# Performance work log

Measured on AMD Instinct MI355X. Metric: run time of the kernel, lower is better.

## Reference

```python
import jax, jax.numpy as jnp
import numpy as np

N, D, NUM_CLASSES = 8192, 512, 100

def _col_normalize(z):
    # torch.std default is unbiased (ddof=1)
    mean = z.mean(axis=0)
    std = z.std(axis=0, ddof=1)
    return (z - mean) / std

def setup_inputs() -> dict:
    key = jax.random.key(0)
    k1, k2, k3 = jax.random.split(key, 3)
    z_a = jax.random.normal(k1, (N, D), dtype=jnp.float32)
    z_b = jax.random.normal(k2, (N, D), dtype=jnp.float32)
    labels = jax.random.randint(k3, (N,), 0, NUM_CLASSES, dtype=jnp.int64)
    return {"z_a": z_a, "z_b": z_b, "labels": labels}

def reference(z_a, z_b, labels):
    d = z_a.shape[1]
    z_a_norm = _col_normalize(z_a)
    z_b_norm = _col_normalize(z_b)
    # c: [N, N] cross-correlation between samples
    c = jnp.matmul(z_a_norm, z_b_norm.T) / d
    # m[i, j] = 1 if labels[i] == labels[j] else 0 (replaces per-row loop)
    m = (labels[:, None] == labels[None, :]).astype(c.dtype)
    loss = jnp.sum((c - m) ** 2)
    return loss
```

## Files before the change

### kernel.cpp

```cpp
#include <hip/hip_runtime.h>
#include <math.h>


#define NN 8192
#define DD 512
#define NC 100
#define SPLITK 16
#define NXT 10
#define NTILE 14

#define GA_B    0u
#define GB_B    1048576u
#define RTA_B   2097152u
#define RTB_B   2359296u
#define MUA_B   2621440u
#define MUB_B   2623488u
#define RSA_B   2625536u
#define RSB_B   2627584u
#define CNT_B   2629632u
#define XTA_B   4194304u
#define XTB_B   12582912u
#define MT_B    20971520u
#define PART_B  23068672u

typedef __attribute__((ext_vector_type(8))) short short8;
typedef __attribute__((ext_vector_type(4))) float f32x4;

__constant__ int c_ti[NTILE] = {0,0,0,0,1,1,1,2,2,3, 0,1,2,3};
__constant__ int c_tj[NTILE] = {0,1,2,3,1,2,3,2,3,3, 4,4,4,4};
__constant__ float c_w[NXT]  = {1.f,2.f,2.f,2.f,1.f,2.f,2.f,1.f,2.f,1.f};

#if defined(__has_builtin)
#if __has_builtin(__builtin_amdgcn_global_load_lds)
#define HAVE_GLL 1
#endif
#endif

#ifdef HAVE_GLL
__device__ __forceinline__ void async16(const void* g, void* l) {
    __builtin_amdgcn_global_load_lds(
        (const __attribute__((address_space(1))) void*)g,
        (__attribute__((address_space(3))) void*)l, 16, 0, 0);
}
#endif

__device__ __forceinline__ short f2bf_rne(float f) {
    unsigned int u = __builtin_bit_cast(unsigned int, f);
    u += 0x7fffu + ((u >> 16) & 1u);
    return (short)(u >> 16);
}

__device__ __forceinline__ float block_reduce_sum(float v) {
    __shared__ float red[8];
    int lane = threadIdx.x & 63;
    int wave = threadIdx.x >> 6;
    #pragma unroll
    for (int off = 32; off > 0; off >>= 1) v += __shfl_down(v, off, 64);
    if (lane == 0) red[wave] = v;
    __syncthreads();
    float s = 0.f;
    if (threadIdx.x == 0) {
        int nw = (blockDim.x + 63) >> 6;
        for (int w = 0; w < nw; w++) s += red[w];
    }
    return s;
}

__global__ void k_init(const int* __restrict__ labels, short* __restrict__ MT,
                       float* __restrict__ out) {
    int c = blockIdx.x;
    if (c == 128) { if (threadIdx.x == 0) out[0] = 0.f; return; }
    int t = threadIdx.x;
    unsigned short one = 0x3F80;
    ushort4* dst = (ushort4*)(MT + (size_t)c * NN);
    const int4* lb4 = (const int4*)labels;
    #pragma unroll
    for (int j = 0; j < 8; j++) {
        int i4 = j * 256 + t;
        int4 lb = lb4[i4];
        ushort4 v;
        v.x = (lb.x == c) ? one : (unsigned short)0;
        v.y = (lb.y == c) ? one : (unsigned short)0;
        v.z = (lb.z == c) ? one : (unsigned short)0;
        v.w = (lb.w == c) ? one : (unsigned short)0;
        dst[i4] = v;
    }
}

__global__ __launch_bounds__(256) void k_convT(const float* __restrict__ A,
                                               const float* __restrict__ B,
                                               short* __restrict__ XTa,
                                               short* __restrict__ XTb) {
    __shared__ short LT[64][72];
    int bid = blockIdx.x;
    const float* X = (bid >> 10) ? B : A;
    short* XT = (bid >> 10) ? XTb : XTa;
    int rem = bid & 1023;
    int c0 = (rem >> 7) << 6;
    int k0 = (rem & 127) << 6;
    int t = threadIdx.x;

    int cc = t & 15;
    int kb = t >> 4;
    #pragma unroll
    for (int s = 0; s < 4; s++) {
        int kr = kb + s * 16;
        float4 v = *(const float4*)&X[(size_t)(k0 + kr) * DD + c0 + cc * 4];
        LT[cc * 4 + 0][kr] = f2bf_rne(v.x);
        LT[cc * 4 + 1][kr] = f2bf_rne(v.y);
        LT[cc * 4 + 2][kr] = f2bf_rne(v.z);
        LT[cc * 4 + 3][kr] = f2bf_rne(v.w);
    }
    __syncthreads();
    #pragma unroll
    for (int s = 0; s < 2; s++) {
        int idx = s * 256 + t;
        int orow = idx >> 3;
        int och = idx & 7;
        *(uint4*)&XT[(size_t)(c0 + orow) * NN + k0 + och * 8] =
            *(const uint4*)&LT[orow][och * 8];
    }
}

__global__ __launch_bounds__(256, 2) void k_gram(const short* __restrict__ XTa,
                                                 const short* __restrict__ XTb,
                                                 const short* __restrict__ MT,
                                                 float* __restrict__ part) {
    __shared__ short LA[128 * 64];
    __shared__ short LB[128 * 64];

    int bid = blockIdx.x;
    int mat = bid / (NTILE * SPLITK);
    int r = bid % (NTILE * SPLITK);
    int chunk = r / NTILE;
    int tile = r % NTILE;
    const short* XT = mat ? XTb : XTa;
    int ti = c_ti[tile], tj = c_tj[tile];
    const short* PA = XT + (size_t)ti * 128 * NN;
    const short* PB = (tj < 4) ? (XT + (size_t)tj * 128 * NN) : MT;
    int k0 = chunk * (NN / SPLITK);

    int t = threadIdx.x;
    int wave = t >> 6, lane = t & 63;
    int quad = lane >> 4, l16 = lane & 15;
    int x7 = l16 & 7;
    int wrow = (wave >> 1) * 64, wcol = (wave & 1) * 64;

    int srow = lane >> 3;
    int sc = (lane & 7) ^ srow;

    f32x4 acc[4][4];
    #pragma unroll
    for (int i = 0; i < 4; i++)
        #pragma unroll
        for (int j = 0; j < 4; j++) acc[i][j] = (f32x4)0.f;

    for (int kk = 0; kk < NN / SPLITK; kk += 64) {
        __syncthreads();
        #pragma unroll
        for (int rr = 0; rr < 4; rr++) {
            int seg = wave * 4 + rr;
            int row = seg * 8 + srow;
            const short* ga = PA + (size_t)row * NN + k0 + kk + sc * 8;
            const short* gb = PB + (size_t)row * NN + k0 + kk + sc * 8;
#ifdef HAVE_GLL
            async16(ga, &LA[seg * 512]);
            async16(gb, &LB[seg * 512]);
#else
            uint4 va = *(const uint4*)ga;
            uint4 vb = *(const uint4*)gb;
            *(uint4*)&LA[seg * 512 + lane * 8] = va;
            *(uint4*)&LB[seg * 512 + lane * 8] = vb;
#endif
        }
        __syncthreads();
        #pragma unroll
        for (int ks = 0; ks < 2; ks++) {
            short8 a[4], b[4];
            #pragma unroll
            for (int mt = 0; mt < 4; mt++)
                a[mt] = *(const short8*)&LA[(wrow + mt * 16 + l16) * 64 +
                                            (((ks * 4 + quad) ^ x7) << 3)];
            #pragma unroll
            for (int nt = 0; nt < 4; nt++)
                b[nt] = *(const short8*)&LB[(wcol + nt * 16 + l16) * 64 +
                                            (((ks * 4 + quad) ^ x7) << 3)];
            #pragma unroll
            for (int mt = 0; mt < 4; mt++)
                #pragma unroll
                for (int nt = 0; nt < 4; nt++)
                    acc[mt][nt] = __builtin_amdgcn_mfma_f32_16x16x32_bf16(
                        a[mt], b[nt], acc[mt][nt], 0, 0, 0);
        }
    }

    float* pbase = part + ((size_t)(mat * NTILE + tile) * SPLITK + chunk) * 16384;
    #pragma unroll
    for (int mt = 0; mt < 4; mt++)
        #pragma unroll
        for (int nt = 0; nt < 4; nt++)
            #pragma unroll
            for (int rj = 0; rj < 4; rj++) {
                int rr2 = wrow + mt * 16 + quad * 4 + rj;
                int cc2 = wcol + nt * 16 + l16;
                pbase[rr2 * 128 + cc2] = acc[mt][nt][rj];
            }
}

__global__ void k_gsum(const float* __restrict__ part,
                       float* __restrict__ Ga, float* __restrict__ Gb,
                       float* __restrict__ RTa, float* __restrict__ RTb) {
    int bid = blockIdx.x;
    int mat = bid / (NTILE * 64);
    int rr = bid % (NTILE * 64);
    int tile = rr / 64;
    int e = (rr % 64) * 256 + threadIdx.x;
    const float* p = part + (size_t)(mat * NTILE + tile) * SPLITK * 16384 + e;
    float s = 0.f;
    #pragma unroll
    for (int c = 0; c < SPLITK; c++) s += p[(size_t)c * 16384];
    int rw = e >> 7, cl = e & 127;
    if (tile < NXT) {
        float* G = mat ? Gb : Ga;
        G[(c_ti[tile] * 128 + rw) * DD + c_tj[tile] * 128 + cl] = s;
    } else {
        float* RT = mat ? RTb : RTa;
        RT[cl * DD + (tile - NXT) * 128 + rw] = s;
    }
}

__global__ void k_stats(const float* __restrict__ Ga, const float* __restrict__ Gb,
                        const float* __restrict__ RTa, const float* __restrict__ RTb,
                        const int* __restrict__ labels,
                        float* mu_a, float* mu_b, float* rs_a, float* rs_b,
                        int* counts) {
    if (blockIdx.x == 2) {
        __shared__ int h[NC];
        int t = threadIdx.x;
        if (t < NC) h[t] = 0;
        __syncthreads();
        for (int i = t; i < NN; i += blockDim.x) atomicAdd(&h[labels[i]], 1);
        __syncthreads();
        if (t < NC) counts[t] = h[t];
        return;
    }
    int mat = blockIdx.x;
    int k = threadIdx.x;
    const float* RT = mat ? RTb : RTa;
    const float* G = mat ? Gb : Ga;
    float s = 0.f;
    for (int c = 0; c < 128; c++) s += RT[c * DD + k];
    float mu = s / (float)NN;
    float sumsq = G[k * DD + k];
    float var = (sumsq - (float)NN * mu * mu) / (float)(NN - 1);
    (mat ? mu_b : mu_a)[k] = mu;
    (mat ? rs_b : rs_a)[k] = rsqrtf(var);
}

__global__ void k_term(const float* __restrict__ Ga, const float* __restrict__ Gb,
                       const float* __restrict__ RTa, const float* __restrict__ RTb,
                       const float* __restrict__ mu_a, const float* __restrict__ mu_b,
                       const float* __restrict__ rs_a, const float* __restrict__ rs_b,
                       const int* __restrict__ counts, float* out) {
    int bid = blockIdx.x;
    if (bid < 256) {
        float local = 0.f;
        for (int x = bid * 256 + threadIdx.x; x < NXT * 16384; x += 256 * 256) {
            int tile = x >> 14, e = x & 16383;
            int gi = c_ti[tile] * 128 + (e >> 7);
            int gj = c_tj[tile] * 128 + (e & 127);
            float ga = rs_a[gi] * rs_a[gj] * (Ga[gi * DD + gj] - (float)NN * mu_a[gi] * mu_a[gj]);
            float gb = rs_b[gi] * rs_b[gj] * (Gb[gi * DD + gj] - (float)NN * mu_b[gi] * mu_b[gj]);
            local += c_w[tile] * ga * gb;
        }
        float s = block_reduce_sum(local);
        if (threadIdx.x == 0) atomicAdd(out, s * (1.0f / ((float)DD * (float)DD)));
    } else {
        int c = bid - 256;
        float n = (float)counts[c];
        float local = 0.f;
        for (int k = threadIdx.x; k < DD; k += 256) {
            float ta = rs_a[k] * (RTa[c * DD + k] - n * mu_a[k]);
            float tb = rs_b[k] * (RTb[c * DD + k] - n * mu_b[k]);
            local += ta * tb;
        }
        float s = block_reduce_sum(local);
        if (threadIdx.x == 0) {
            float add = s * (-2.0f / (float)DD);
            if (c == 0) {
                float t3 = 0.f;
                for (int cc = 0; cc < NC; cc++) {
                    float nc = (float)counts[cc];
                    t3 += nc * nc;
                }
                add += t3;
            }
            atomicAdd(out, add);
        }
    }
}

extern "C" void kernel_launch(void* const* d_in, const int* in_sizes, int n_in,
                              void* d_out, int out_size, void* d_ws, size_t ws_size,
                              hipStream_t stream) {
    const float* z_a = (const float*)d_in[0];
    const float* z_b = (const float*)d_in[1];
    const int* labels = (const int*)d_in[2];
    float* out = (float*)d_out;
    char* wsb = (char*)d_ws;

    float* Ga = (float*)(wsb + GA_B);
    float* Gb = (float*)(wsb + GB_B);
    float* RTa = (float*)(wsb + RTA_B);
    float* RTb = (float*)(wsb + RTB_B);
    float* mu_a = (float*)(wsb + MUA_B);
    float* mu_b = (float*)(wsb + MUB_B);
    float* rs_a = (float*)(wsb + RSA_B);
    float* rs_b = (float*)(wsb + RSB_B);
    int* counts = (int*)(wsb + CNT_B);
    short* XTa = (short*)(wsb + XTA_B);
    short* XTb = (short*)(wsb + XTB_B);
    short* MT = (short*)(wsb + MT_B);
    float* part = (float*)(wsb + PART_B);

    hipLaunchKernelGGL(k_init, dim3(129), dim3(256), 0, stream, labels, MT, out);
    hipLaunchKernelGGL(k_convT, dim3(2048), dim3(256), 0, stream, z_a, z_b, XTa, XTb);
    hipLaunchKernelGGL(k_gram, dim3(2 * NTILE * SPLITK), dim3(256), 0, stream,
                       XTa, XTb, MT, part);
    hipLaunchKernelGGL(k_gsum, dim3(2 * NTILE * 64), dim3(256), 0, stream,
                       part, Ga, Gb, RTa, RTb);
    hipLaunchKernelGGL(k_stats, dim3(3), dim3(512), 0, stream,
                       Ga, Gb, RTa, RTb, labels, mu_a, mu_b, rs_a, rs_b, counts);
    hipLaunchKernelGGL(k_term, dim3(356), dim3(256), 0, stream,
                       Ga, Gb, RTa, RTb, mu_a, mu_b, rs_a, rs_b, counts, out);
}
```

Measured before the change: 118.3 us.

## Fold split-K reduction into consumers and compute column sums during transpose

Removes the k_gsum pass: k_stats reads the diagonal partials straight from the split-K buffer, and k_term sums the SPLITK partials inline, with the Gram work spread over more blocks. Column sums for the means are now gathered in k_convT with shared and global atomics, and the label histogram moves into k_init. This drops one launch and the write and re-read of the G and RT matrices. In exchange k_convT uses strided scalar loads with no LDS transpose, and the float atomics make the column sums order-dependent.

```diff
diff --git a/kernel.cpp b/kernel.cpp
--- a/kernel.cpp
+++ b/kernel.cpp
@@ -9,15 +9,12 @@
 #define NXT 10
 #define NTILE 14
 
-#define GA_B    0u
-#define GB_B    1048576u
-#define RTA_B   2097152u
-#define RTB_B   2359296u
-#define MUA_B   2621440u
-#define MUB_B   2623488u
-#define RSA_B   2625536u
-#define RSB_B   2627584u
-#define CNT_B   2629632u
+#define MUA_B   0u
+#define MUB_B   2048u
+#define RSA_B   4096u
+#define RSB_B   6144u
+#define CNT_B   8192u
+#define CS_B    12288u
 #define XTA_B   4194304u
 #define XTB_B   12582912u
 #define MT_B    20971520u
@@ -44,10 +41,10 @@
 }
 #endif
 
-__device__ __forceinline__ short f2bf_rne(float f) {
+__device__ __forceinline__ unsigned short f2bf_rne(float f) {
     unsigned int u = __builtin_bit_cast(unsigned int, f);
     u += 0x7fffu + ((u >> 16) & 1u);
-    return (short)(u >> 16);
+    return (unsigned short)(u >> 16);
 }
 
 __device__ __forceinline__ float block_reduce_sum(float v) {
@@ -67,10 +64,24 @@
 }
 
 __global__ void k_init(const int* __restrict__ labels, short* __restrict__ MT,
+                       float* __restrict__ colsum, int* __restrict__ counts,
                        float* __restrict__ out) {
     int c = blockIdx.x;
-    if (c == 128) { if (threadIdx.x == 0) out[0] = 0.f; return; }
     int t = threadIdx.x;
+    if (c == 128) {
+        __shared__ int h[NC];
+        if (t < NC) h[t] = 0;
+        __syncthreads();
+        for (int i = t; i < NN; i += blockDim.x) atomicAdd(&h[labels[i]], 1);
+        __syncthreads();
+        if (t < NC) counts[t] = h[t];
+        return;
+    }
+    if (c == 129) {
+        for (int i = t; i < 2 * DD; i += blockDim.x) colsum[i] = 0.f;
+        if (t == 0) out[0] = 0.f;
+        return;
+    }
     unsigned short one = 0x3F80;
     ushort4* dst = (ushort4*)(MT + (size_t)c * NN);
     const int4* lb4 = (const int4*)labels;
@@ -90,36 +101,42 @@
 __global__ __launch_bounds__(256) void k_convT(const float* __restrict__ A,
                                                const float* __restrict__ B,
                                                short* __restrict__ XTa,
-                                               short* __restrict__ XTb) {
-    __shared__ short LT[64][72];
-    int bid = blockIdx.x;
-    const float* X = (bid >> 10) ? B : A;
-    short* XT = (bid >> 10) ? XTb : XTa;
-    int rem = bid & 1023;
-    int c0 = (rem >> 7) << 6;
-    int k0 = (rem & 127) << 6;
+                                               short* __restrict__ XTb,
+                                               float* __restrict__ colsum) {
+    int b = blockIdx.x;
+    int mat = b >> 9;
+    int cg = (b >> 6) & 7;
+    int kg = b & 63;
+    const float* X = mat ? B : A;
+    short* XT = mat ? XTb : XTa;
     int t = threadIdx.x;
-
-    int cc = t & 15;
-    int kb = t >> 4;
-    #pragma unroll
-    for (int s = 0; s < 4; s++) {
-        int kr = kb + s * 16;
-        float4 v = *(const float4*)&X[(size_t)(k0 + kr) * DD + c0 + cc * 4];
-        LT[cc * 4 + 0][kr] = f2bf_rne(v.x);
-        LT[cc * 4 + 1][kr] = f2bf_rne(v.y);
-        LT[cc * 4 + 2][kr] = f2bf_rne(v.z);
-        LT[cc * 4 + 3][kr] = f2bf_rne(v.w);
-    }
+    int cl = t & 63;
+    int c = cg * 64 + cl;
+    int k0 = kg * 128 + (t >> 6) * 32;
+
+    const float* src = X + (size_t)k0 * DD + c;
+    short* dst = XT + (size_t)c * NN + k0;
+    float s = 0.f;
+    #pragma unroll
+    for (int j = 0; j < 4; j++) {
+        unsigned int w[4];
+        #pragma unroll
+        for (int q = 0; q < 4; q++) {
+            float v0 = src[(size_t)(j * 8 + q * 2) * DD];
+            float v1 = src[(size_t)(j * 8 + q * 2 + 1) * DD];
+            s += v0 + v1;
+            w[q] = ((unsigned int)f2bf_rne(v1) << 16) | (unsigned int)f2bf_rne(v0);
+        }
+        uint4 vv; vv.x = w[0]; vv.y = w[1]; vv.z = w[2]; vv.w = w[3];
+        *(uint4*)(dst + j * 8) = vv;
+    }
+
+    __shared__ float cs[64];
+    if (t < 64) cs[t] = 0.f;
     __syncthreads();
-    #pragma unroll
-    for (int s = 0; s < 2; s++) {
-        int idx = s * 256 + t;
-        int orow = idx >> 3;
-        int och = idx & 7;
-        *(uint4*)&XT[(size_t)(c0 + orow) * NN + k0 + och * 8] =
-            *(const uint4*)&LT[orow][och * 8];
-    }
+    atomicAdd(&cs[cl], s);
+    __syncthreads();
+    if (t < 64) atomicAdd(&colsum[mat * DD + cg * 64 + t], cs[t]);
 }
 
 __global__ __launch_bounds__(256, 2) void k_gram(const short* __restrict__ XTa,
@@ -207,85 +224,73 @@
             }
 }
 
-__global__ void k_gsum(const float* __restrict__ part,
-                       float* __restrict__ Ga, float* __restrict__ Gb,
-                       float* __restrict__ RTa, float* __restrict__ RTb) {
-    int bid = blockIdx.x;
-    int mat = bid / (NTILE * 64);
-    int rr = bid % (NTILE * 64);
-    int tile = rr / 64;
-    int e = (rr % 64) * 256 + threadIdx.x;
-    const float* p = part + (size_t)(mat * NTILE + tile) * SPLITK * 16384 + e;
-    float s = 0.f;
-    #pragma unroll
-    for (int c = 0; c < SPLITK; c++) s += p[(size_t)c * 16384];
-    int rw = e >> 7, cl = e & 127;
-    if (tile < NXT) {
-        float* G = mat ? Gb : Ga;
-        G[(c_ti[tile] * 128 + rw) * DD + c_tj[tile] * 128 + cl] = s;
-    } else {
-        float* RT = mat ? RTb : RTa;
-        RT[cl * DD + (tile - NXT) * 128 + rw] = s;
-    }
-}
-
-__global__ void k_stats(const float* __restrict__ Ga, const float* __restrict__ Gb,
-                        const float* __restrict__ RTa, const float* __restrict__ RTb,
-                        const int* __restrict__ labels,
-                        float* mu_a, float* mu_b, float* rs_a, float* rs_b,
-                        int* counts) {
-    if (blockIdx.x == 2) {
-        __shared__ int h[NC];
-        int t = threadIdx.x;
-        if (t < NC) h[t] = 0;
-        __syncthreads();
-        for (int i = t; i < NN; i += blockDim.x) atomicAdd(&h[labels[i]], 1);
-        __syncthreads();
-        if (t < NC) counts[t] = h[t];
-        return;
-    }
+__global__ void k_stats(const float* __restrict__ part, const float* __restrict__ colsum,
+                        float* mu_a, float* mu_b, float* rs_a, float* rs_b) {
     int mat = blockIdx.x;
     int k = threadIdx.x;
-    const float* RT = mat ? RTb : RTa;
-    const float* G = mat ? Gb : Ga;
-    float s = 0.f;
-    for (int c = 0; c < 128; c++) s += RT[c * DD + k];
-    float mu = s / (float)NN;
-    float sumsq = G[k * DD + k];
+    const int dmap[4] = {0, 4, 7, 9};
+    int tile = dmap[k >> 7];
+    size_t base = ((size_t)(mat * NTILE + tile) * SPLITK) * 16384 + (size_t)(k & 127) * 129;
+    float sumsq = 0.f;
+    #pragma unroll
+    for (int c = 0; c < SPLITK; c++) sumsq += part[base + (size_t)c * 16384];
+    float mu = colsum[mat * DD + k] / (float)NN;
     float var = (sumsq - (float)NN * mu * mu) / (float)(NN - 1);
     (mat ? mu_b : mu_a)[k] = mu;
     (mat ? rs_b : rs_a)[k] = rsqrtf(var);
 }
 
-__global__ void k_term(const float* __restrict__ Ga, const float* __restrict__ Gb,
-                       const float* __restrict__ RTa, const float* __restrict__ RTb,
+__global__ void k_term(const float* __restrict__ part,
                        const float* __restrict__ mu_a, const float* __restrict__ mu_b,
                        const float* __restrict__ rs_a, const float* __restrict__ rs_b,
                        const int* __restrict__ counts, float* out) {
     int bid = blockIdx.x;
-    if (bid < 256) {
+    int t = threadIdx.x;
+    if (bid < 320) {
+        int tile = bid >> 5;
+        int seg = bid & 31;
+        size_t baseA = ((size_t)(0 * NTILE + tile) * SPLITK) * 16384;
+        size_t baseB = ((size_t)(1 * NTILE + tile) * SPLITK) * 16384;
+        float w = c_w[tile];
         float local = 0.f;
-        for (int x = bid * 256 + threadIdx.x; x < NXT * 16384; x += 256 * 256) {
-            int tile = x >> 14, e = x & 16383;
+        #pragma unroll
+        for (int half = 0; half < 2; half++) {
+            int e = seg * 512 + half * 256 + t;
+            float sA = 0.f, sB = 0.f;
+            #pragma unroll
+            for (int c = 0; c < SPLITK; c++) {
+                sA += part[baseA + (size_t)c * 16384 + e];
+                sB += part[baseB + (size_t)c * 16384 + e];
+            }
             int gi = c_ti[tile] * 128 + (e >> 7);
             int gj = c_tj[tile] * 128 + (e & 127);
-            float ga = rs_a[gi] * rs_a[gj] * (Ga[gi * DD + gj] - (float)NN * mu_a[gi] * mu_a[gj]);
-            float gb = rs_b[gi] * rs_b[gj] * (Gb[gi * DD + gj] - (float)NN * mu_b[gi] * mu_b[gj]);
-            local += c_w[tile] * ga * gb;
+            float ga = rs_a[gi] * rs_a[gj] * (sA - (float)NN * mu_a[gi] * mu_a[gj]);
+            float gb = rs_b[gi] * rs_b[gj] * (sB - (float)NN * mu_b[gi] * mu_b[gj]);
+            local += w * ga * gb;
         }
         float s = block_reduce_sum(local);
-        if (threadIdx.x == 0) atomicAdd(out, s * (1.0f / ((float)DD * (float)DD)));
+        if (t == 0) atomicAdd(out, s * (1.0f / ((float)DD * (float)DD)));
     } else {
-        int c = bid - 256;
+        int c = bid - 320;
         float n = (float)counts[c];
         float local = 0.f;
-        for (int k = threadIdx.x; k < DD; k += 256) {
-            float ta = rs_a[k] * (RTa[c * DD + k] - n * mu_a[k]);
-            float tb = rs_b[k] * (RTb[c * DD + k] - n * mu_b[k]);
+        for (int k = t; k < DD; k += 256) {
+            int tile = NXT + (k >> 7);
+            size_t e = (size_t)(k & 127) * 128 + c;
+            size_t baseA = ((size_t)(0 * NTILE + tile) * SPLITK) * 16384 + e;
+            size_t baseB = ((size_t)(1 * NTILE + tile) * SPLITK) * 16384 + e;
+            float sA = 0.f, sB = 0.f;
+            #pragma unroll
+            for (int ch = 0; ch < SPLITK; ch++) {
+                sA += part[baseA + (size_t)ch * 16384];
+                sB += part[baseB + (size_t)ch * 16384];
+            }
+            float ta = rs_a[k] * (sA - n * mu_a[k]);
+            float tb = rs_b[k] * (sB - n * mu_b[k]);
             local += ta * tb;
         }
         float s = block_reduce_sum(local);
-        if (threadIdx.x == 0) {
+        if (t == 0) {
             float add = s * (-2.0f / (float)DD);
             if (c == 0) {
                 float t3 = 0.f;
@@ -309,28 +314,25 @@
     float* out = (float*)d_out;
     char* wsb = (char*)d_ws;
 
-    float* Ga = (float*)(wsb + GA_B);
-    float* Gb = (float*)(wsb + GB_B);
-    float* RTa = (float*)(wsb + RTA_B);
-    float* RTb = (float*)(wsb + RTB_B);
     float* mu_a = (float*)(wsb + MUA_B);
     float* mu_b = (float*)(wsb + MUB_B);
     float* rs_a = (float*)(wsb + RSA_B);
     float* rs_b = (float*)(wsb + RSB_B);
     int* counts = (int*)(wsb + CNT_B);
+    float* colsum = (float*)(wsb + CS_B);
     short* XTa = (short*)(wsb + XTA_B);
     short* XTb = (short*)(wsb + XTB_B);
     short* MT = (short*)(wsb + MT_B);
     float* part = (float*)(wsb + PART_B);
 
-    hipLaunchKernelGGL(k_init, dim3(129), dim3(256), 0, stream, labels, MT, out);
-    hipLaunchKernelGGL(k_convT, dim3(2048), dim3(256), 0, stream, z_a, z_b, XTa, XTb);
+    hipLaunchKernelGGL(k_init, dim3(130), dim3(256), 0, stream,
+                       labels, MT, colsum, counts, out);
+    hipLaunchKernelGGL(k_convT, dim3(1024), dim3(256), 0, stream,
+                       z_a, z_b, XTa, XTb, colsum);
     hipLaunchKernelGGL(k_gram, dim3(2 * NTILE * SPLITK), dim3(256), 0, stream,
                        XTa, XTb, MT, part);
-    hipLaunchKernelGGL(k_gsum, dim3(2 * NTILE * 64), dim3(256), 0, stream,
-                       part, Ga, Gb, RTa, RTb);
-    hipLaunchKernelGGL(k_stats, dim3(3), dim3(512), 0, stream,
-                       Ga, Gb, RTa, RTb, labels, mu_a, mu_b, rs_a, rs_b, counts);
-    hipLaunchKernelGGL(k_term, dim3(356), dim3(256), 0, stream,
-                       Ga, Gb, RTa, RTb, mu_a, mu_b, rs_a, rs_b, counts, out);
-}
+    hipLaunchKernelGGL(k_stats, dim3(2), dim3(512), 0, stream,
+                       part, colsum, mu_a, mu_b, rs_a, rs_b);
+    hipLaunchKernelGGL(k_term, dim3(420), dim3(256), 0, stream,
+                       part, mu_a, mu_b, rs_a, rs_b, counts, out);
+}
```

Measured after the change: 145.0 us. 22.6% more time.

## Fuse all stages into one cooperative persistent kernel with grid syncs

Applied to the files above, without the earlier changes.

Replaces the six separate launches (init, transpose-convert, gram, split-K reduce, stats, loss terms) with one cooperative kernel of 448 blocks. Stages are separated by grid.sync(), and the earlier stages use grid-stride job loops. The aim is to remove per-launch gaps and tail idle time between the small stages. The trade-offs are the cost of several grid-wide barriers and a larger LDS footprint per block from combining all stages. The Gram term loop now walks the full 512x512 matrix and skips the lower triangle, instead of using the tile table.

```diff
diff --git a/kernel.cpp b/kernel.cpp
--- a/kernel.cpp
+++ b/kernel.cpp
@@ -1,5 +1,8 @@
 #include <hip/hip_runtime.h>
+#include <hip/hip_cooperative_groups.h>
 #include <math.h>
+
+namespace cg = cooperative_groups;
 
 
 #define NN 8192
@@ -8,6 +11,7 @@
 #define SPLITK 16
 #define NXT 10
 #define NTILE 14
+#define GRID 448
 
 #define GA_B    0u
 #define GB_B    1048576u
@@ -44,10 +48,10 @@
 }
 #endif
 
-__device__ __forceinline__ short f2bf_rne(float f) {
+__device__ __forceinline__ unsigned short f2bf_rne(float f) {
     unsigned int u = __builtin_bit_cast(unsigned int, f);
     u += 0x7fffu + ((u >> 16) & 1u);
-    return (short)(u >> 16);
+    return (unsigned short)(u >> 16);
 }
 
 __device__ __forceinline__ float block_reduce_sum(float v) {
@@ -66,226 +70,221 @@
     return s;
 }
 
-__global__ void k_init(const int* __restrict__ labels, short* __restrict__ MT,
-                       float* __restrict__ out) {
-    int c = blockIdx.x;
-    if (c == 128) { if (threadIdx.x == 0) out[0] = 0.f; return; }
-    int t = threadIdx.x;
-    unsigned short one = 0x3F80;
-    ushort4* dst = (ushort4*)(MT + (size_t)c * NN);
-    const int4* lb4 = (const int4*)labels;
-    #pragma unroll
-    for (int j = 0; j < 8; j++) {
-        int i4 = j * 256 + t;
-        int4 lb = lb4[i4];
-        ushort4 v;
-        v.x = (lb.x == c) ? one : (unsigned short)0;
-        v.y = (lb.y == c) ? one : (unsigned short)0;
-        v.z = (lb.z == c) ? one : (unsigned short)0;
-        v.w = (lb.w == c) ? one : (unsigned short)0;
-        dst[i4] = v;
-    }
-}
-
-__global__ __launch_bounds__(256) void k_convT(const float* __restrict__ A,
-                                               const float* __restrict__ B,
-                                               short* __restrict__ XTa,
-                                               short* __restrict__ XTb) {
+__global__ __launch_bounds__(256, 2) void k_fused(
+        const float* __restrict__ A, const float* __restrict__ B,
+        const int* __restrict__ labels,
+        short* __restrict__ XTa, short* __restrict__ XTb, short* __restrict__ MT,
+        float* __restrict__ part,
+        float* __restrict__ Ga, float* __restrict__ Gb,
+        float* __restrict__ RTa, float* __restrict__ RTb,
+        float* __restrict__ mu_a, float* __restrict__ mu_b,
+        float* __restrict__ rs_a, float* __restrict__ rs_b,
+        int* __restrict__ counts, float* __restrict__ out) {
+    cg::grid_group grid = cg::this_grid();
     __shared__ short LT[64][72];
-    int bid = blockIdx.x;
-    const float* X = (bid >> 10) ? B : A;
-    short* XT = (bid >> 10) ? XTb : XTa;
-    int rem = bid & 1023;
-    int c0 = (rem >> 7) << 6;
-    int k0 = (rem & 127) << 6;
-    int t = threadIdx.x;
-
-    int cc = t & 15;
-    int kb = t >> 4;
-    #pragma unroll
-    for (int s = 0; s < 4; s++) {
-        int kr = kb + s * 16;
-        float4 v = *(const float4*)&X[(size_t)(k0 + kr) * DD + c0 + cc * 4];
-        LT[cc * 4 + 0][kr] = f2bf_rne(v.x);
-        LT[cc * 4 + 1][kr] = f2bf_rne(v.y);
-        LT[cc * 4 + 2][kr] = f2bf_rne(v.z);
-        LT[cc * 4 + 3][kr] = f2bf_rne(v.w);
-    }
-    __syncthreads();
-    #pragma unroll
-    for (int s = 0; s < 2; s++) {
-        int idx = s * 256 + t;
-        int orow = idx >> 3;
-        int och = idx & 7;
-        *(uint4*)&XT[(size_t)(c0 + orow) * NN + k0 + och * 8] =
-            *(const uint4*)&LT[orow][och * 8];
-    }
-}
-
-__global__ __launch_bounds__(256, 2) void k_gram(const short* __restrict__ XTa,
-                                                 const short* __restrict__ XTb,
-                                                 const short* __restrict__ MT,
-                                                 float* __restrict__ part) {
     __shared__ short LA[128 * 64];
     __shared__ short LB[128 * 64];
 
-    int bid = blockIdx.x;
-    int mat = bid / (NTILE * SPLITK);
-    int r = bid % (NTILE * SPLITK);
-    int chunk = r / NTILE;
-    int tile = r % NTILE;
-    const short* XT = mat ? XTb : XTa;
-    int ti = c_ti[tile], tj = c_tj[tile];
-    const short* PA = XT + (size_t)ti * 128 * NN;
-    const short* PB = (tj < 4) ? (XT + (size_t)tj * 128 * NN) : MT;
-    int k0 = chunk * (NN / SPLITK);
-
-    int t = threadIdx.x;
-    int wave = t >> 6, lane = t & 63;
-    int quad = lane >> 4, l16 = lane & 15;
-    int x7 = l16 & 7;
-    int wrow = (wave >> 1) * 64, wcol = (wave & 1) * 64;
-
-    int srow = lane >> 3;
-    int sc = (lane & 7) ^ srow;
-
-    f32x4 acc[4][4];
-    #pragma unroll
-    for (int i = 0; i < 4; i++)
+    const int bid = blockIdx.x;
+    const int t = threadIdx.x;
+
+    for (int job = bid; job < 2177; job += GRID) {
+        if (job < 2048) {
+            int mat = job >> 10;
+            const float* X = mat ? B : A;
+            short* XT = mat ? XTb : XTa;
+            int rem = job & 1023;
+            int c0 = (rem >> 7) << 6;
+            int k0 = (rem & 127) << 6;
+            int cc = t & 15;
+            int kb = t >> 4;
+            #pragma unroll
+            for (int s = 0; s < 4; s++) {
+                int kr = kb + s * 16;
+                float4 v = *(const float4*)&X[(size_t)(k0 + kr) * DD + c0 + cc * 4];
+                LT[cc * 4 + 0][kr] = (short)f2bf_rne(v.x);
+                LT[cc * 4 + 1][kr] = (short)f2bf_rne(v.y);
+                LT[cc * 4 + 2][kr] = (short)f2bf_rne(v.z);
+                LT[cc * 4 + 3][kr] = (short)f2bf_rne(v.w);
+            }
+            __syncthreads();
+            #pragma unroll
+            for (int s = 0; s < 2; s++) {
+                int idx = s * 256 + t;
+                int orow = idx >> 3;
+                int och = idx & 7;
+                *(uint4*)&XT[(size_t)(c0 + orow) * NN + k0 + och * 8] =
+                    *(const uint4*)&LT[orow][och * 8];
+            }
+            __syncthreads();
+        } else if (job < 2176) {
+            int c = job - 2048;
+            unsigned short one = 0x3F80;
+            ushort4* dst = (ushort4*)(MT + (size_t)c * NN);
+            const int4* lb4 = (const int4*)labels;
+            #pragma unroll
+            for (int j = 0; j < 8; j++) {
+                int i4 = j * 256 + t;
+                int4 lb = lb4[i4];
+                ushort4 v;
+                v.x = (lb.x == c) ? one : (unsigned short)0;
+                v.y = (lb.y == c) ? one : (unsigned short)0;
+                v.z = (lb.z == c) ? one : (unsigned short)0;
+                v.w = (lb.w == c) ? one : (unsigned short)0;
+                dst[i4] = v;
+            }
+        } else {
+            if (t == 0) out[0] = 0.f;
+        }
+    }
+    grid.sync();
+
+    {
+        int mat = bid / (NTILE * SPLITK);
+        int r = bid % (NTILE * SPLITK);
+        int chunk = r / NTILE;
+        int tile = r % NTILE;
+        const short* XT = mat ? XTb : XTa;
+        int ti = c_ti[tile], tj = c_tj[tile];
+        const short* PA = XT + (size_t)ti * 128 * NN;
+        const short* PB = (tj < 4) ? (XT + (size_t)tj * 128 * NN) : MT;
+        int k0 = chunk * (NN / SPLITK);
+
+        int wave = t >> 6, lane = t & 63;
+        int quad = lane >> 4, l16 = lane & 15;
+        int x7 = l16 & 7;
+        int wrow = (wave >> 1) * 64, wcol = (wave & 1) * 64;
+
+        int srow = lane >> 3;
+        int sc = (lane & 7) ^ srow;
+
+        f32x4 acc[4][4];
         #pragma unroll
-        for (int j = 0; j < 4; j++) acc[i][j] = (f32x4)0.f;
-
-    for (int kk = 0; kk < NN / SPLITK; kk += 64) {
-        __syncthreads();
-        #pragma unroll
-        for (int rr = 0; rr < 4; rr++) {
-            int seg = wave * 4 + rr;
-            int row = seg * 8 + srow;
-            const short* ga = PA + (size_t)row * NN + k0 + kk + sc * 8;
-            const short* gb = PB + (size_t)row * NN + k0 + kk + sc * 8;
+        for (int i = 0; i < 4; i++)
+            #pragma unroll
+            for (int j = 0; j < 4; j++) acc[i][j] = (f32x4)0.f;
+
+        for (int kk = 0; kk < NN / SPLITK; kk += 64) {
+            __syncthreads();
+            #pragma unroll
+            for (int rr = 0; rr < 4; rr++) {
+                int seg = wave * 4 + rr;
+                int row = seg * 8 + srow;
+                const short* ga = PA + (size_t)row * NN + k0 + kk + sc * 8;
+                const short* gb = PB + (size_t)row * NN + k0 + kk + sc * 8;
 #ifdef HAVE_GLL
-            async16(ga, &LA[seg * 512]);
-            async16(gb, &LB[seg * 512]);
+                async16(ga, &LA[seg * 512]);
+                async16(gb, &LB[seg * 512]);
 #else
-            uint4 va = *(const uint4*)ga;
-            uint4 vb = *(const uint4*)gb;
-            *(uint4*)&LA[seg * 512 + lane * 8] = va;
-            *(uint4*)&LB[seg * 512 + lane * 8] = vb;
+                uint4 va = *(const uint4*)ga;
+                uint4 vb = *(const uint4*)gb;
+                *(uint4*)&LA[seg * 512 + lane * 8] = va;
+                *(uint4*)&LB[seg * 512 + lane * 8] = vb;
 #endif
-        }
-        __syncthreads();
-        #pragma unroll
-        for (int ks = 0; ks < 2; ks++) {
-            short8 a[4], b[4];
-            #pragma unroll
-            for (int mt = 0; mt < 4; mt++)
-                a[mt] = *(const short8*)&LA[(wrow + mt * 16 + l16) * 64 +
-                                            (((ks * 4 + quad) ^ x7) << 3)];
-            #pragma unroll
-            for (int nt = 0; nt < 4; nt++)
-                b[nt] = *(const short8*)&LB[(wcol + nt * 16 + l16) * 64 +
-                                            (((ks * 4 + quad) ^ x7) << 3)];
-            #pragma unroll
-            for (int mt = 0; mt < 4; mt++)
+            }
+            __syncthreads();
+            #pragma unroll
+            for (int ks = 0; ks < 2; ks++) {
+                short8 a[4], b[4];
+                #pragma unroll
+                for (int mt = 0; mt < 4; mt++)
+                    a[mt] = *(const short8*)&LA[(wrow + mt * 16 + l16) * 64 +
+                                                (((ks * 4 + quad) ^ x7) << 3)];
                 #pragma unroll
                 for (int nt = 0; nt < 4; nt++)
-                    acc[mt][nt] = __builtin_amdgcn_mfma_f32_16x16x32_bf16(
-                        a[mt], b[nt], acc[mt][nt], 0, 0, 0);
-        }
-    }
-
-    float* pbase = part + ((size_t)(mat * NTILE + tile) * SPLITK + chunk) * 16384;
-    #pragma unroll
-    for (int mt = 0; mt < 4; mt++)
+                    b[nt] = *(const short8*)&LB[(wcol + nt * 16 + l16) * 64 +
+                                                (((ks * 4 + quad) ^ x7) << 3)];
+                #pragma unroll
+                for (int mt = 0; mt < 4; mt++)
+                    #pragma unroll
+                    for (int nt = 0; nt < 4; nt++)
+                        acc[mt][nt] = __builtin_amdgcn_mfma_f32_16x16x32_bf16(
+                            a[mt], b[nt], acc[mt][nt], 0, 0, 0);
+            }
+        }
+
+        float* pbase = part + ((size_t)(mat * NTILE + tile) * SPLITK + chunk) * 16384;
         #pragma unroll
-        for (int nt = 0; nt < 4; nt++)
-            #pragma unroll
-            for (int rj = 0; rj < 4; rj++) {
-                int rr2 = wrow + mt * 16 + quad * 4 + rj;
-                int cc2 = wcol + nt * 16 + l16;
-                pbase[rr2 * 128 + cc2] = acc[mt][nt][rj];
-            }
-}
-
-__global__ void k_gsum(const float* __restrict__ part,
-                       float* __restrict__ Ga, float* __restrict__ Gb,
-                       float* __restrict__ RTa, float* __restrict__ RTb) {
-    int bid = blockIdx.x;
-    int mat = bid / (NTILE * 64);
-    int rr = bid % (NTILE * 64);
-    int tile = rr / 64;
-    int e = (rr % 64) * 256 + threadIdx.x;
-    const float* p = part + (size_t)(mat * NTILE + tile) * SPLITK * 16384 + e;
-    float s = 0.f;
-    #pragma unroll
-    for (int c = 0; c < SPLITK; c++) s += p[(size_t)c * 16384];
-    int rw = e >> 7, cl = e & 127;
-    if (tile < NXT) {
-        float* G = mat ? Gb : Ga;
-        G[(c_ti[tile] * 128 + rw) * DD + c_tj[tile] * 128 + cl] = s;
-    } else {
-        float* RT = mat ? RTb : RTa;
-        RT[cl * DD + (tile - NXT) * 128 + rw] = s;
-    }
-}
-
-__global__ void k_stats(const float* __restrict__ Ga, const float* __restrict__ Gb,
-                        const float* __restrict__ RTa, const float* __restrict__ RTb,
-                        const int* __restrict__ labels,
-                        float* mu_a, float* mu_b, float* rs_a, float* rs_b,
-                        int* counts) {
-    if (blockIdx.x == 2) {
-        __shared__ int h[NC];
-        int t = threadIdx.x;
-        if (t < NC) h[t] = 0;
-        __syncthreads();
-        for (int i = t; i < NN; i += blockDim.x) atomicAdd(&h[labels[i]], 1);
-        __syncthreads();
-        if (t < NC) counts[t] = h[t];
-        return;
-    }
-    int mat = blockIdx.x;
-    int k = threadIdx.x;
-    const float* RT = mat ? RTb : RTa;
-    const float* G = mat ? Gb : Ga;
-    float s = 0.f;
-    for (int c = 0; c < 128; c++) s += RT[c * DD + k];
-    float mu = s / (float)NN;
-    float sumsq = G[k * DD + k];
-    float var = (sumsq - (float)NN * mu * mu) / (float)(NN - 1);
-    (mat ? mu_b : mu_a)[k] = mu;
-    (mat ? rs_b : rs_a)[k] = rsqrtf(var);
-}
-
-__global__ void k_term(const float* __restrict__ Ga, const float* __restrict__ Gb,
-                       const float* __restrict__ RTa, const float* __restrict__ RTb,
-                       const float* __restrict__ mu_a, const float* __restrict__ mu_b,
-                       const float* __restrict__ rs_a, const float* __restrict__ rs_b,
-                       const int* __restrict__ counts, float* out) {
-    int bid = blockIdx.x;
+        for (int mt = 0; mt < 4; mt++)
+            #pragma unroll
+            for (int nt = 0; nt < 4; nt++)
+                #pragma unroll
+                for (int rj = 0; rj < 4; rj++) {
+                    int rr2 = wrow + mt * 16 + quad * 4 + rj;
+                    int cc2 = wcol + nt * 16 + l16;
+                    pbase[rr2 * 128 + cc2] = acc[mt][nt][rj];
+                }
+    }
+    grid.sync();
+
+    for (int job = bid; job < 2 * NTILE * 64; job += GRID) {
+        int mat = job / (NTILE * 64);
+        int rr = job % (NTILE * 64);
+        int tile = rr / 64;
+        int e = (rr % 64) * 256 + t;
+        const float* p = part + (size_t)(mat * NTILE + tile) * SPLITK * 16384 + e;
+        float s = 0.f;
+        #pragma unroll
+        for (int c = 0; c < SPLITK; c++) s += p[(size_t)c * 16384];
+        int rw = e >> 7, cl = e & 127;
+        if (tile < NXT) {
+            float* G = mat ? Gb : Ga;
+            G[(c_ti[tile] * 128 + rw) * DD + c_tj[tile] * 128 + cl] = s;
+        } else {
+            float* RT = mat ? RTb : RTa;
+            RT[cl * DD + (tile - NXT) * 128 + rw] = s;
+        }
+    }
+    grid.sync();
+
+    if (bid < 3) {
+        if (bid == 2) {
+            __shared__ int h[NC];
+            if (t < NC) h[t] = 0;
+            __syncthreads();
+            for (int i = t; i < NN; i += 256) atomicAdd(&h[labels[i]], 1);
+            __syncthreads();
+            if (t < NC) counts[t] = h[t];
+        } else {
+            int mat = bid;
+            const float* RT = mat ? RTb : RTa;
+            const float* G = mat ? Gb : Ga;
+            for (int k = t; k < DD; k += 256) {
+                float s = 0.f;
+                for (int c = 0; c < 128; c++) s += RT[c * DD + k];
+                float mu = s / (float)NN;
+                float sumsq = G[k * DD + k];
+                float var = (sumsq - (float)NN * mu * mu) / (float)(NN - 1);
+                (mat ? mu_b : mu_a)[k] = mu;
+                (mat ? rs_b : rs_a)[k] = rsqrtf(var);
+            }
+        }
+    }
+    grid.sync();
+
     if (bid < 256) {
         float local = 0.f;
-        for (int x = bid * 256 + threadIdx.x; x < NXT * 16384; x += 256 * 256) {
-            int tile = x >> 14, e = x & 16383;
-            int gi = c_ti[tile] * 128 + (e >> 7);
-            int gj = c_tj[tile] * 128 + (e & 127);
-            float ga = rs_a[gi] * rs_a[gj] * (Ga[gi * DD + gj] - (float)NN * mu_a[gi] * mu_a[gj]);
-            float gb = rs_b[gi] * rs_b[gj] * (Gb[gi * DD + gj] - (float)NN * mu_b[gi] * mu_b[gj]);
-            local += c_w[tile] * ga * gb;
+        for (int x = bid * 256 + t; x < DD * DD; x += 256 * 256) {
+            int k = x >> 9, l = x & (DD - 1);
+            if (l < k) continue;
+            float w = (l == k) ? 1.f : 2.f;
+            float ga = rs_a[k] * rs_a[l] * (Ga[x] - (float)NN * mu_a[k] * mu_a[l]);
+            float gb = rs_b[k] * rs_b[l] * (Gb[x] - (float)NN * mu_b[k] * mu_b[l]);
+            local += w * ga * gb;
         }
         float s = block_reduce_sum(local);
-        if (threadIdx.x == 0) atomicAdd(out, s * (1.0f / ((float)DD * (float)DD)));
-    } else {
+        if (t == 0) atomicAdd(out, s * (1.0f / ((float)DD * (float)DD)));
+    } else if (bid < 256 + NC) {
         int c = bid - 256;
         float n = (float)counts[c];
         float local = 0.f;
-        for (int k = threadIdx.x; k < DD; k += 256) {
+        for (int k = t; k < DD; k += 256) {
             float ta = rs_a[k] * (RTa[c * DD + k] - n * mu_a[k]);
             float tb = rs_b[k] * (RTb[c * DD + k] - n * mu_b[k]);
             local += ta * tb;
         }
         float s = block_reduce_sum(local);
-        if (threadIdx.x == 0) {
+        if (t == 0) {
             float add = s * (-2.0f / (float)DD);
             if (c == 0) {
                 float t3 = 0.f;
@@ -323,14 +322,13 @@
     short* MT = (short*)(wsb + MT_B);
     float* part = (float*)(wsb + PART_B);
 
-    hipLaunchKernelGGL(k_init, dim3(129), dim3(256), 0, stream, labels, MT, out);
-    hipLaunchKernelGGL(k_convT, dim3(2048), dim3(256), 0, stream, z_a, z_b, XTa, XTb);
-    hipLaunchKernelGGL(k_gram, dim3(2 * NTILE * SPLITK), dim3(256), 0, stream,
-                       XTa, XTb, MT, part);
-    hipLaunchKernelGGL(k_gsum, dim3(2 * NTILE * 64), dim3(256), 0, stream,
-                       part, Ga, Gb, RTa, RTb);
-    hipLaunchKernelGGL(k_stats, dim3(3), dim3(512), 0, stream,
-                       Ga, Gb, RTa, RTb, labels, mu_a, mu_b, rs_a, rs_b, counts);
-    hipLaunchKernelGGL(k_term, dim3(356), dim3(256), 0, stream,
-                       Ga, Gb, RTa, RTb, mu_a, mu_b, rs_a, rs_b, counts, out);
-}
+    void* kargs[] = {
+        (void*)&z_a, (void*)&z_b, (void*)&labels,
+        (void*)&XTa, (void*)&XTb, (void*)&MT, (void*)&part,
+        (void*)&Ga, (void*)&Gb, (void*)&RTa, (void*)&RTb,
+        (void*)&mu_a, (void*)&mu_b, (void*)&rs_a, (void*)&rs_b,
+        (void*)&counts, (void*)&out
+    };
+    hipLaunchCooperativeKernel((void*)k_fused, dim3(GRID), dim3(256),
+                               kargs, 0, stream);
+}
```

Measured after the change: 351.0 us. +196.6%, slower.

## Fold init and stats kernels into convT and gram, compute column stats early

Applied to the files above, without the earlier changes.

The label-mask build moves into extra blocks of the transpose/convert kernel, which now also accumulates fp32 per-column sums and sums of squares into per-block partials. Extra blocks in the gram kernel reduce those partials into means and inverse stds, build the label histogram and zero the output. This removes two launches and the serial stats kernel from the critical path. The term kernel now walks the full 512x512 index space and skips the lower triangle, so half its threads idle, and the LDS atomics add a little work to convT.

```diff
diff --git a/kernel.cpp b/kernel.cpp
--- a/kernel.cpp
+++ b/kernel.cpp
@@ -18,6 +18,8 @@
 #define RSA_B   2625536u
 #define RSB_B   2627584u
 #define CNT_B   2629632u
+#define CPS_B   2630656u
+#define CPQ_B   3154944u
 #define XTA_B   4194304u
 #define XTB_B   12582912u
 #define MT_B    20971520u
@@ -28,7 +30,6 @@
 
 __constant__ int c_ti[NTILE] = {0,0,0,0,1,1,1,2,2,3, 0,1,2,3};
 __constant__ int c_tj[NTILE] = {0,1,2,3,1,2,3,2,3,3, 4,4,4,4};
-__constant__ float c_w[NXT]  = {1.f,2.f,2.f,2.f,1.f,2.f,2.f,1.f,2.f,1.f};
 
 #if defined(__has_builtin)
 #if __has_builtin(__builtin_amdgcn_global_load_lds)
@@ -44,10 +45,10 @@
 }
 #endif
 
-__device__ __forceinline__ short f2bf_rne(float f) {
+__device__ __forceinline__ unsigned short f2bf_rne(float f) {
     unsigned int u = __builtin_bit_cast(unsigned int, f);
     u += 0x7fffu + ((u >> 16) & 1u);
-    return (short)(u >> 16);
+    return (unsigned short)(u >> 16);
 }
 
 __device__ __forceinline__ float block_reduce_sum(float v) {
@@ -66,50 +67,63 @@
     return s;
 }
 
-__global__ void k_init(const int* __restrict__ labels, short* __restrict__ MT,
-                       float* __restrict__ out) {
-    int c = blockIdx.x;
-    if (c == 128) { if (threadIdx.x == 0) out[0] = 0.f; return; }
-    int t = threadIdx.x;
-    unsigned short one = 0x3F80;
-    ushort4* dst = (ushort4*)(MT + (size_t)c * NN);
-    const int4* lb4 = (const int4*)labels;
-    #pragma unroll
-    for (int j = 0; j < 8; j++) {
-        int i4 = j * 256 + t;
-        int4 lb = lb4[i4];
-        ushort4 v;
-        v.x = (lb.x == c) ? one : (unsigned short)0;
-        v.y = (lb.y == c) ? one : (unsigned short)0;
-        v.z = (lb.z == c) ? one : (unsigned short)0;
-        v.w = (lb.w == c) ? one : (unsigned short)0;
-        dst[i4] = v;
-    }
-}
-
 __global__ __launch_bounds__(256) void k_convT(const float* __restrict__ A,
                                                const float* __restrict__ B,
+                                               const int* __restrict__ labels,
                                                short* __restrict__ XTa,
-                                               short* __restrict__ XTb) {
+                                               short* __restrict__ XTb,
+                                               short* __restrict__ MT,
+                                               float* __restrict__ cps,
+                                               float* __restrict__ cpq) {
+    int bid = blockIdx.x;
+    int t = threadIdx.x;
+
+    if (bid >= 2048) {
+        int c = bid - 2048;
+        unsigned short one = 0x3F80;
+        ushort4* dst = (ushort4*)(MT + (size_t)c * NN);
+        const int4* lb4 = (const int4*)labels;
+        #pragma unroll
+        for (int j = 0; j < 8; j++) {
+            int i4 = j * 256 + t;
+            int4 lb = lb4[i4];
+            ushort4 v;
+            v.x = (lb.x == c) ? one : (unsigned short)0;
+            v.y = (lb.y == c) ? one : (unsigned short)0;
+            v.z = (lb.z == c) ? one : (unsigned short)0;
+            v.w = (lb.w == c) ? one : (unsigned short)0;
+            dst[i4] = v;
+        }
+        return;
+    }
+
     __shared__ short LT[64][72];
-    int bid = blockIdx.x;
-    const float* X = (bid >> 10) ? B : A;
-    short* XT = (bid >> 10) ? XTb : XTa;
+    __shared__ float cs[64], cq[64];
+    int mat = bid >> 10;
+    const float* X = mat ? B : A;
+    short* XT = mat ? XTb : XTa;
     int rem = bid & 1023;
-    int c0 = (rem >> 7) << 6;
-    int k0 = (rem & 127) << 6;
-    int t = threadIdx.x;
+    int cgrp = rem >> 7;
+    int kgrp = rem & 127;
+    int c0 = cgrp << 6;
+    int k0 = kgrp << 6;
+
+    if (t < 64) { cs[t] = 0.f; cq[t] = 0.f; }
 
     int cc = t & 15;
     int kb = t >> 4;
+    float a0 = 0.f, a1 = 0.f, a2 = 0.f, a3 = 0.f;
+    float q0 = 0.f, q1 = 0.f, q2 = 0.f, q3 = 0.f;
     #pragma unroll
     for (int s = 0; s < 4; s++) {
         int kr = kb + s * 16;
         float4 v = *(const float4*)&X[(size_t)(k0 + kr) * DD + c0 + cc * 4];
-        LT[cc * 4 + 0][kr] = f2bf_rne(v.x);
-        LT[cc * 4 + 1][kr] = f2bf_rne(v.y);
-        LT[cc * 4 + 2][kr] = f2bf_rne(v.z);
-        LT[cc * 4 + 3][kr] = f2bf_rne(v.w);
+        a0 += v.x; a1 += v.y; a2 += v.z; a3 += v.w;
+        q0 += v.x * v.x; q1 += v.y * v.y; q2 += v.z * v.z; q3 += v.w * v.w;
+        LT[cc * 4 + 0][kr] = (short)f2bf_rne(v.x);
+        LT[cc * 4 + 1][kr] = (short)f2bf_rne(v.y);
+        LT[cc * 4 + 2][kr] = (short)f2bf_rne(v.z);
+        LT[cc * 4 + 3][kr] = (short)f2bf_rne(v.w);
     }
     __syncthreads();
     #pragma unroll
@@ -120,16 +134,65 @@
         *(uint4*)&XT[(size_t)(c0 + orow) * NN + k0 + och * 8] =
             *(const uint4*)&LT[orow][och * 8];
     }
+    atomicAdd(&cs[cc * 4 + 0], a0); atomicAdd(&cq[cc * 4 + 0], q0);
+    atomicAdd(&cs[cc * 4 + 1], a1); atomicAdd(&cq[cc * 4 + 1], q1);
+    atomicAdd(&cs[cc * 4 + 2], a2); atomicAdd(&cq[cc * 4 + 2], q2);
+    atomicAdd(&cs[cc * 4 + 3], a3); atomicAdd(&cq[cc * 4 + 3], q3);
+    __syncthreads();
+    if (t < 64) {
+        size_t slot = ((size_t)(mat * 8 + cgrp) * 128 + kgrp) * 64 + t;
+        cps[slot] = cs[t];
+        cpq[slot] = cq[t];
+    }
 }
 
 __global__ __launch_bounds__(256, 2) void k_gram(const short* __restrict__ XTa,
                                                  const short* __restrict__ XTb,
                                                  const short* __restrict__ MT,
-                                                 float* __restrict__ part) {
+                                                 const int* __restrict__ labels,
+                                                 const float* __restrict__ cps,
+                                                 const float* __restrict__ cpq,
+                                                 float* __restrict__ part,
+                                                 float* __restrict__ mu_a,
+                                                 float* __restrict__ mu_b,
+                                                 float* __restrict__ rs_a,
+                                                 float* __restrict__ rs_b,
+                                                 int* __restrict__ counts,
+                                                 float* __restrict__ out) {
+    int bid = blockIdx.x;
+    int t = threadIdx.x;
+
+    if (bid >= 448) {
+        if (bid == 448) {
+            __shared__ int h[NC];
+            if (t < NC) h[t] = 0;
+            __syncthreads();
+            for (int i = t; i < NN; i += 256) atomicAdd(&h[labels[i]], 1);
+            __syncthreads();
+            if (t < NC) counts[t] = h[t];
+            if (t == 0) out[0] = 0.f;
+        } else {
+            int mat = bid - 449;
+            for (int k = t; k < DD; k += 256) {
+                int cg = k >> 6, cl = k & 63;
+                size_t base = ((size_t)(mat * 8 + cg) * 128) * 64 + cl;
+                float s = 0.f, sq = 0.f;
+                for (int kg = 0; kg < 128; kg++) {
+                    s  += cps[base + (size_t)kg * 64];
+                    sq += cpq[base + (size_t)kg * 64];
+                }
+                float mu = s / (float)NN;
+                float var = (sq - (float)NN * mu * mu) / (float)(NN - 1);
+                (mat ? mu_b : mu_a)[k] = mu;
+                (mat ? rs_b : rs_a)[k] = rsqrtf(var);
+            }
+        }
+        return;
+    }
+
     __shared__ short LA[128 * 64];
     __shared__ short LB[128 * 64];
 
-    int bid = blockIdx.x;
     int mat = bid / (NTILE * SPLITK);
     int r = bid % (NTILE * SPLITK);
     int chunk = r / NTILE;
@@ -140,7 +203,6 @@
     const short* PB = (tj < 4) ? (XT + (size_t)tj * 128 * NN) : MT;
     int k0 = chunk * (NN / SPLITK);
 
-    int t = threadIdx.x;
     int wave = t >> 6, lane = t & 63;
     int quad = lane >> 4, l16 = lane & 15;
     int x7 = l16 & 7;
@@ -229,63 +291,36 @@
     }
 }
 
-__global__ void k_stats(const float* __restrict__ Ga, const float* __restrict__ Gb,
-                        const float* __restrict__ RTa, const float* __restrict__ RTb,
-                        const int* __restrict__ labels,
-                        float* mu_a, float* mu_b, float* rs_a, float* rs_b,
-                        int* counts) {
-    if (blockIdx.x == 2) {
-        __shared__ int h[NC];
-        int t = threadIdx.x;
-        if (t < NC) h[t] = 0;
-        __syncthreads();
-        for (int i = t; i < NN; i += blockDim.x) atomicAdd(&h[labels[i]], 1);
-        __syncthreads();
-        if (t < NC) counts[t] = h[t];
-        return;
-    }
-    int mat = blockIdx.x;
-    int k = threadIdx.x;
-    const float* RT = mat ? RTb : RTa;
-    const float* G = mat ? Gb : Ga;
-    float s = 0.f;
-    for (int c = 0; c < 128; c++) s += RT[c * DD + k];
-    float mu = s / (float)NN;
-    float sumsq = G[k * DD + k];
-    float var = (sumsq - (float)NN * mu * mu) / (float)(NN - 1);
-    (mat ? mu_b : mu_a)[k] = mu;
-    (mat ? rs_b : rs_a)[k] = rsqrtf(var);
-}
-
 __global__ void k_term(const float* __restrict__ Ga, const float* __restrict__ Gb,
                        const float* __restrict__ RTa, const float* __restrict__ RTb,
                        const float* __restrict__ mu_a, const float* __restrict__ mu_b,
                        const float* __restrict__ rs_a, const float* __restrict__ rs_b,
                        const int* __restrict__ counts, float* out) {
     int bid = blockIdx.x;
+    int t = threadIdx.x;
     if (bid < 256) {
         float local = 0.f;
-        for (int x = bid * 256 + threadIdx.x; x < NXT * 16384; x += 256 * 256) {
-            int tile = x >> 14, e = x & 16383;
-            int gi = c_ti[tile] * 128 + (e >> 7);
-            int gj = c_tj[tile] * 128 + (e & 127);
-            float ga = rs_a[gi] * rs_a[gj] * (Ga[gi * DD + gj] - (float)NN * mu_a[gi] * mu_a[gj]);
-            float gb = rs_b[gi] * rs_b[gj] * (Gb[gi * DD + gj] - (float)NN * mu_b[gi] * mu_b[gj]);
-            local += c_w[tile] * ga * gb;
+        for (int x = bid * 256 + t; x < DD * DD; x += 256 * 256) {
+            int k = x >> 9, l = x & (DD - 1);
+            if (l < k) continue;
+            float w = (l == k) ? 1.f : 2.f;
+            float ga = rs_a[k] * rs_a[l] * (Ga[x] - (float)NN * mu_a[k] * mu_a[l]);
+            float gb = rs_b[k] * rs_b[l] * (Gb[x] - (float)NN * mu_b[k] * mu_b[l]);
+            local += w * ga * gb;
         }
         float s = block_reduce_sum(local);
-        if (threadIdx.x == 0) atomicAdd(out, s * (1.0f / ((float)DD * (float)DD)));
+        if (t == 0) atomicAdd(out, s * (1.0f / ((float)DD * (float)DD)));
     } else {
         int c = bid - 256;
         float n = (float)counts[c];
         float local = 0.f;
-        for (int k = threadIdx.x; k < DD; k += 256) {
+        for (int k = t; k < DD; k += 256) {
             float ta = rs_a[k] * (RTa[c * DD + k] - n * mu_a[k]);
             float tb = rs_b[k] * (RTb[c * DD + k] - n * mu_b[k]);
             local += ta * tb;
         }
         float s = block_reduce_sum(local);
-        if (threadIdx.x == 0) {
+        if (t == 0) {
             float add = s * (-2.0f / (float)DD);
             if (c == 0) {
                 float t3 = 0.f;
@@ -318,19 +353,20 @@
     float* rs_a = (float*)(wsb + RSA_B);
     float* rs_b = (float*)(wsb + RSB_B);
     int* counts = (int*)(wsb + CNT_B);
+    float* cps = (float*)(wsb + CPS_B);
+    float* cpq = (float*)(wsb + CPQ_B);
     short* XTa = (short*)(wsb + XTA_B);
     short* XTb = (short*)(wsb + XTB_B);
     short* MT = (short*)(wsb + MT_B);
     float* part = (float*)(wsb + PART_B);
 
-    hipLaunchKernelGGL(k_init, dim3(129), dim3(256), 0, stream, labels, MT, out);
-    hipLaunchKernelGGL(k_convT, dim3(2048), dim3(256), 0, stream, z_a, z_b, XTa, XTb);
-    hipLaunchKernelGGL(k_gram, dim3(2 * NTILE * SPLITK), dim3(256), 0, stream,
-                       XTa, XTb, MT, part);
+    hipLaunchKernelGGL(k_convT, dim3(2176), dim3(256), 0, stream,
+                       z_a, z_b, labels, XTa, XTb, MT, cps, cpq);
+    hipLaunchKernelGGL(k_gram, dim3(451), dim3(256), 0, stream,
+                       XTa, XTb, MT, labels, cps, cpq, part,
+                       mu_a, mu_b, rs_a, rs_b, counts, out);
     hipLaunchKernelGGL(k_gsum, dim3(2 * NTILE * 64), dim3(256), 0, stream,
                        part, Ga, Gb, RTa, RTb);
-    hipLaunchKernelGGL(k_stats, dim3(3), dim3(512), 0, stream,
-                       Ga, Gb, RTa, RTb, labels, mu_a, mu_b, rs_a, rs_b, counts);
     hipLaunchKernelGGL(k_term, dim3(356), dim3(256), 0, stream,
                        Ga, Gb, RTa, RTb, mu_a, mu_b, rs_a, rs_b, counts, out);
 }
```

Result: slower. 131.5 us (+11.1%).
